# Kernel tuning notes

Hardware: AMD Instinct MI355X
Metric: run time of the kernel (lower is better)

## Reference

```python
import jax, jax.numpy as jnp
import numpy as np

N_HEAD = 8
DQK = 64
DV = 64
D_IN = 512
D_OUT = 512
D_MID = 2048
B = 4
L = 2048
EPS = 1e-5


def layernorm(x):
    mu = jnp.mean(x, axis=-1, keepdims=True)
    var = jnp.mean(jnp.square(x - mu), axis=-1, keepdims=True)
    return (x - mu) / jnp.sqrt(var + EPS)


def setup_inputs() -> dict:
    key = jax.random.key(0)
    ks = jax.random.split(key, 10)
    s = 0.02
    return {
        "query": jax.random.normal(ks[0], (B, L, D_IN), jnp.float32),
        "key": jax.random.normal(ks[1], (B, L, D_IN), jnp.float32),
        "value": jax.random.normal(ks[2], (B, L, D_IN), jnp.float32),
        "mask": jnp.zeros((B, L, L), jnp.float32),
        "WQ": jax.random.normal(ks[3], (D_IN, N_HEAD * DQK), jnp.float32) * s,
        "WK": jax.random.normal(ks[4], (D_IN, N_HEAD * DQK), jnp.float32) * s,
        "WV": jax.random.normal(ks[5], (D_IN, N_HEAD * DV), jnp.float32) * s,
        "WO": jax.random.normal(ks[6], (N_HEAD * DV, D_OUT), jnp.float32) * s,
        "W1": jax.random.normal(ks[7], (D_OUT, D_MID), jnp.float32) * s,
        "W2": jax.random.normal(ks[8], (D_MID, D_OUT), jnp.float32) * s,
    }


def reference(query, key, value, mask, WQ, WK, WV, WO, W1, W2):
    bsz = query.shape[0]
    # projections -> [b, h, l, d]
    Q = (query @ WQ).reshape(bsz, -1, N_HEAD, DQK).transpose(0, 2, 1, 3)
    K = (key @ WK).reshape(bsz, -1, N_HEAD, DQK).transpose(0, 2, 1, 3)
    V = (value @ WV).reshape(bsz, -1, N_HEAD, DV).transpose(0, 2, 1, 3)
    # scaled dot-product attention with additive mask [b, 1, lq, lk]
    scores = jnp.einsum("bhqd,bhkd->bhqk", Q, K) / jnp.sqrt(jnp.float32(DQK))
    w = jax.nn.softmax(scores + mask[:, None, :, :], axis=-1)
    out = jnp.einsum("bhqk,bhkd->bhqd", w, V)
    out = out.transpose(0, 2, 1, 3).reshape(bsz, -1, N_HEAD * DV)
    out = out @ WO
    out = layernorm(query + out)
    ff = jax.nn.relu(out @ W1) @ W2
    return layernorm(out + ff)
```

## Files before the change

kernel.cpp:

```cpp
#include <hip/hip_runtime.h>
#include <hip/hip_bf16.h>

using bf16 = __bf16;
typedef __bf16 bf16x4 __attribute__((ext_vector_type(4)));
typedef __bf16 bf16x8 __attribute__((ext_vector_type(8)));
typedef float f32x4 __attribute__((ext_vector_type(4)));

static constexpr int BATCH = 4;
static constexpr int SEQ   = 2048;
static constexpr int DIN   = 512;
static constexpr int NHEAD = 8;
static constexpr int DMID  = 2048;
static constexpr int MROWS = BATCH * SEQ;

__device__ __forceinline__ void gload16(const void* g, void* l)
{
    __builtin_amdgcn_global_load_lds(
        (const __attribute__((address_space(1))) unsigned int*)g,
        (__attribute__((address_space(3))) unsigned int*)l, 16, 0, 0);
}

__device__ __forceinline__ bf16x4 ds_tr16(const bf16* p)
{
    bf16x4 r;
    auto lp = (const __attribute__((address_space(3))) bf16*)p;
    asm volatile("ds_read_b64_tr_b16 %0, %1" : "=&v"(r) : "v"(lp) : "memory");
    return r;
}

__global__ __launch_bounds__(256) void tw_mask(
    const float* __restrict__ WQ, const float* __restrict__ WK,
    const float* __restrict__ WV, const float* __restrict__ WO,
    const float* __restrict__ W1, const float* __restrict__ W2,
    bf16* __restrict__ WQt, bf16* __restrict__ WKt, bf16* __restrict__ WVt,
    bf16* __restrict__ WOt, bf16* __restrict__ W1t, bf16* __restrict__ W2t,
    const float* __restrict__ q, const float* __restrict__ k,
    const float* __restrict__ v,
    bf16* __restrict__ qb, bf16* __restrict__ kb, bf16* __restrict__ vb,
    const uint4* __restrict__ mask, int* __restrict__ flag)
{
    const int bid = blockIdx.x;
    if (bid >= 4096) {
        const int idx = bid - 4096;
        const float* src = idx < 1024 ? q : idx < 2048 ? k : v;
        bf16*       dst = idx < 1024 ? qb : idx < 2048 ? kb : vb;
        const size_t b4 = (size_t)(idx & 1023) * 1024;
#pragma unroll
        for (int i = 0; i < 4; ++i) {
            const float4 f = reinterpret_cast<const float4*>(src)[b4 + i * 256 + threadIdx.x];
            bf16x4 h;
            h[0] = (bf16)f.x; h[1] = (bf16)f.y; h[2] = (bf16)f.z; h[3] = (bf16)f.w;
            reinterpret_cast<bf16x4*>(dst)[b4 + i * 256 + threadIdx.x] = h;
        }
        return;
    }
    if (bid >= 3072) {
        const uint4* p = mask + (size_t)(bid - 3072) * 4096;
        unsigned nz = 0;
#pragma unroll
        for (int i = 0; i < 16; ++i) {
            const uint4 u = p[i * 256 + threadIdx.x];
            nz |= u.x | u.y | u.z | u.w;
        }
        if (nz) atomicOr(flag, 1);
        return;
    }
    __shared__ float tile[32][33];
    const float* in; bf16* out; int ip, op, cx, ry;
    if (bid < 1024) {
        const int w = bid >> 8, idx = bid & 255;
        in  = w == 0 ? WQ  : w == 1 ? WK  : w == 2 ? WV  : WO;
        out = w == 0 ? WQt : w == 1 ? WKt : w == 2 ? WVt : WOt;
        ip = 512; op = 512; cx = idx & 15; ry = idx >> 4;
    } else if (bid < 2048) {
        const int idx = bid - 1024;
        in = W1; out = W1t; ip = 2048; op = 512; cx = idx & 63; ry = idx >> 6;
    } else {
        const int idx = bid - 2048;
        in = W2; out = W2t; ip = 512; op = 2048; cx = idx & 15; ry = idx >> 4;
    }
    const int c0 = cx * 32, r0 = ry * 32;
    const int tx = threadIdx.x & 31, ty = threadIdx.x >> 5;
    for (int i = 0; i < 32; i += 8)
        tile[ty + i][tx] = in[(size_t)(r0 + ty + i) * ip + c0 + tx];
    __syncthreads();
    for (int i = 0; i < 32; i += 8)
        out[(size_t)(c0 + ty + i) * op + r0 + tx] = (bf16)tile[tx][ty + i];
}

template <int ACT>
__global__ __launch_bounds__(256) void gemm128(const bf16* __restrict__ A,
                                               const bf16* __restrict__ Bt,
                                               bf16* __restrict__ C,
                                               int N, int K)
{
    __shared__ bf16 sA[128 * 64];
    __shared__ bf16 sB[128 * 64];

    const int t    = threadIdx.x;
    const int lane = t & 63;
    const int wave = t >> 6;
    const int wm   = wave >> 1;
    const int wn   = wave & 1;
    const int lr   = lane & 15;
    const int lq   = lane >> 4;

    const int m0 = blockIdx.y * 128;
    const int n0 = blockIdx.x * 128;

    const int srow = lane >> 3;
    const int scol = (lane & 7) * 8;

    f32x4 acc[4][4] = {};

    for (int k0 = 0; k0 < K; k0 += 64) {
        if (k0) __syncthreads();
#pragma unroll
        for (int i = 0; i < 4; ++i) {
            const int ch = wave * 4 + i;
            const int r  = ch * 8 + srow;
            gload16(A  + (size_t)(m0 + r) * K + k0 + scol, sA + ch * 512);
            gload16(Bt + (size_t)(n0 + r) * K + k0 + scol, sB + ch * 512);
        }
        __syncthreads();

#pragma unroll
        for (int kk = 0; kk < 2; ++kk) {
            bf16x8 af[4], bfr[4];
#pragma unroll
            for (int x = 0; x < 4; ++x) {
                af[x]  = *reinterpret_cast<const bf16x8*>(&sA[(wm * 64 + x * 16 + lr) * 64 + kk * 32 + lq * 8]);
                bfr[x] = *reinterpret_cast<const bf16x8*>(&sB[(wn * 64 + x * 16 + lr) * 64 + kk * 32 + lq * 8]);
            }
#pragma unroll
            for (int m = 0; m < 4; ++m)
#pragma unroll
                for (int n = 0; n < 4; ++n)
                    acc[m][n] = __builtin_amdgcn_mfma_f32_16x16x32_bf16(af[m], bfr[n], acc[m][n], 0, 0, 0);
        }
    }

#pragma unroll
    for (int n = 0; n < 4; ++n) {
        const int col = n0 + wn * 64 + n * 16 + lr;
#pragma unroll
        for (int m = 0; m < 4; ++m) {
            const int rowb = m0 + wm * 64 + m * 16 + lq * 4;
#pragma unroll
            for (int j = 0; j < 4; ++j) {
                float v = acc[m][n][j];
                if (ACT == 1) v = v > 0.f ? v : 0.f;
                C[(size_t)(rowb + j) * N + col] = (bf16)v;
            }
        }
    }
}

__global__ __launch_bounds__(256) void gemm64_qkvb(const bf16* __restrict__ qb,
                                                   const bf16* __restrict__ kb,
                                                   const bf16* __restrict__ vb,
                                                   const bf16* __restrict__ WQt,
                                                   const bf16* __restrict__ WKt,
                                                   const bf16* __restrict__ WVt,
                                                   bf16* __restrict__ Qb,
                                                   bf16* __restrict__ Kb,
                                                   bf16* __restrict__ Vt)
{
    __shared__ bf16 sA[64 * 64];
    __shared__ bf16 sB[128 * 64];

    const bf16* A  = blockIdx.z == 0 ? qb  : blockIdx.z == 1 ? kb  : vb;
    const bf16* Bt = blockIdx.z == 0 ? WQt : blockIdx.z == 1 ? WKt : WVt;
    const int K = DIN;

    const int t    = threadIdx.x;
    const int lane = t & 63;
    const int wave = t >> 6;
    const int lr   = lane & 15;
    const int lq   = lane >> 4;

    const int m0 = blockIdx.y * 64;
    const int n0 = blockIdx.x * 128;

    const int srow = lane >> 3;
    const int scol = (lane & 7) * 8;

    f32x4 acc[4][2] = {};

    for (int k0 = 0; k0 < K; k0 += 64) {
        if (k0) __syncthreads();
#pragma unroll
        for (int i = 0; i < 2; ++i) {
            const int ch = wave * 2 + i;
            gload16(A + (size_t)(m0 + ch * 8 + srow) * K + k0 + scol, sA + ch * 512);
        }
#pragma unroll
        for (int i = 0; i < 4; ++i) {
            const int ch = wave * 4 + i;
            gload16(Bt + (size_t)(n0 + ch * 8 + srow) * K + k0 + scol, sB + ch * 512);
        }
        __syncthreads();

#pragma unroll
        for (int kk = 0; kk < 2; ++kk) {
            bf16x8 af[4], bfr[2];
#pragma unroll
            for (int x = 0; x < 4; ++x)
                af[x] = *reinterpret_cast<const bf16x8*>(&sA[(x * 16 + lr) * 64 + kk * 32 + lq * 8]);
#pragma unroll
            for (int n = 0; n < 2; ++n)
                bfr[n] = *reinterpret_cast<const bf16x8*>(&sB[(wave * 32 + n * 16 + lr) * 64 + kk * 32 + lq * 8]);
#pragma unroll
            for (int m = 0; m < 4; ++m)
#pragma unroll
                for (int n = 0; n < 2; ++n)
                    acc[m][n] = __builtin_amdgcn_mfma_f32_16x16x32_bf16(af[m], bfr[n], acc[m][n], 0, 0, 0);
        }
    }

    if (blockIdx.z < 2) {
        bf16* C = blockIdx.z == 0 ? Qb : Kb;
#pragma unroll
        for (int n = 0; n < 2; ++n) {
            const int col = n0 + wave * 32 + n * 16 + lr;
#pragma unroll
            for (int m = 0; m < 4; ++m) {
                const int rowb = m0 + m * 16 + lq * 4;
#pragma unroll
                for (int j = 0; j < 4; ++j)
                    C[(size_t)(rowb + j) * DIN + col] = (bf16)acc[m][n][j];
            }
        }
    } else {
        __syncthreads();
#pragma unroll
        for (int n = 0; n < 2; ++n)
#pragma unroll
            for (int m = 0; m < 4; ++m)
#pragma unroll
                for (int j = 0; j < 4; ++j)
                    sB[(wave * 32 + n * 16 + lr) * 64 + m * 16 + lq * 4 + j] = (bf16)acc[m][n][j];
        __syncthreads();
        const int c = t >> 1, half = t & 1;
#pragma unroll
        for (int qq = 0; qq < 4; ++qq) {
            const bf16x8 vv = *reinterpret_cast<const bf16x8*>(&sB[c * 64 + half * 32 + qq * 8]);
            *reinterpret_cast<bf16x8*>(Vt + (size_t)(n0 + c) * MROWS + m0 + half * 32 + qq * 8) = vv;
        }
    }
}

__global__ __launch_bounds__(256) void attn_kernel(const bf16* __restrict__ Qb,
                                                   const bf16* __restrict__ Kb,
                                                   const bf16* __restrict__ Vt,
                                                   const float* __restrict__ mask,
                                                   bf16* __restrict__ O,
                                                   const int* __restrict__ mzf)
{
    const int bi   = blockIdx.x;
    const int xcd  = bi & 7;
    const int slot = bi >> 3;
    const int pair = xcd * 4 + (slot >> 4);
    const int qt   = slot & 15;
    const int h    = pair >> 2;
    const int b    = pair & 3;

    const int t    = threadIdx.x;
    const int lane = t & 63;
    const int wave = t >> 6;
    const int lr   = lane & 15;
    const int lq   = lane >> 4;
    const int q0   = qt * 128;
    const bool useM = (*mzf != 0);

    __shared__ bf16 sK[64 * 72];
    __shared__ bf16 sV[64 * 72];
    __shared__ bf16 sPT[4][2048];
    __shared__ bf16 sM[128 * 68];

    bf16x8 qf[2][2];
#pragma unroll
    for (int g = 0; g < 2; ++g) {
        const int qrow = q0 + wave * 32 + g * 16 + lr;
        const bf16* qp = Qb + (size_t)(b * SEQ + qrow) * DIN + h * 64 + lq * 8;
        qf[g][0] = *reinterpret_cast<const bf16x8*>(qp);
        qf[g][1] = *reinterpret_cast<const bf16x8*>(qp + 32);
    }

    f32x4 o[2][4] = {};
    f32x4 lrow[2] = {};

    const int sr = t >> 2;
    const int sc = (t & 3) << 3;

    const bf16*  kbase = Kb + (size_t)(b * SEQ) * DIN + h * 64;
    const bf16*  vbase = Vt + (size_t)(h * 64 + sr) * MROWS + b * SEQ;
    const float* mbase = mask + ((size_t)b * SEQ + q0) * SEQ;

    constexpr float L2E = 1.4426950408889634f;
    constexpr float SCL = 0.125f * L2E;
    const bf16x8 ones = {(bf16)1.f, (bf16)1.f, (bf16)1.f, (bf16)1.f,
                         (bf16)1.f, (bf16)1.f, (bf16)1.f, (bf16)1.f};

    int4 kr0 = *reinterpret_cast<const int4*>(kbase + (size_t)sr * DIN + sc);
    int4 kr1 = *reinterpret_cast<const int4*>(kbase + (size_t)sr * DIN + sc + 32);
    int4 vr0 = *reinterpret_cast<const int4*>(vbase + sc);
    int4 vr1 = *reinterpret_cast<const int4*>(vbase + sc + 32);

    for (int tile = 0; tile < SEQ / 64; ++tile) {
        if (tile) __syncthreads();

        *reinterpret_cast<int4*>(&sK[sr * 72 + sc])      = kr0;
        *reinterpret_cast<int4*>(&sK[sr * 72 + sc + 32]) = kr1;
        *reinterpret_cast<int4*>(&sV[sr * 72 + sc])      = vr0;
        *reinterpret_cast<int4*>(&sV[sr * 72 + sc + 32]) = vr1;
        if (useM) {
            const int k0 = tile * 64;
#pragma unroll
            for (int i = 0; i < 8; ++i) {
                const int idx = t + 256 * i;
                const float4 mr = *reinterpret_cast<const float4*>(
                    mbase + (size_t)(idx >> 4) * SEQ + k0 + (idx & 15) * 4);
                bf16x4 mv;
                mv[0] = (bf16)(mr.x * L2E); mv[1] = (bf16)(mr.y * L2E);
                mv[2] = (bf16)(mr.z * L2E); mv[3] = (bf16)(mr.w * L2E);
                *reinterpret_cast<bf16x4*>(&sM[(idx >> 4) * 68 + (idx & 15) * 4]) = mv;
            }
        }

        if (tile + 1 < SEQ / 64) {
            const int k0 = (tile + 1) * 64;
            kr0 = *reinterpret_cast<const int4*>(kbase + (size_t)(k0 + sr) * DIN + sc);
            kr1 = *reinterpret_cast<const int4*>(kbase + (size_t)(k0 + sr) * DIN + sc + 32);
            vr0 = *reinterpret_cast<const int4*>(vbase + k0 + sc);
            vr1 = *reinterpret_cast<const int4*>(vbase + k0 + sc + 32);
        }
        __syncthreads();

        bf16x8 kf[2][4];
#pragma unroll
        for (int s = 0; s < 2; ++s)
#pragma unroll
            for (int ni = 0; ni < 4; ++ni)
                kf[s][ni] = *reinterpret_cast<const bf16x8*>(&sK[(ni * 16 + lr) * 72 + s * 32 + lq * 8]);

#pragma unroll
        for (int g = 0; g < 2; ++g) {
            f32x4 sf[4] = {};
            __builtin_amdgcn_s_setprio(1);
#pragma unroll
            for (int s = 0; s < 2; ++s)
#pragma unroll
                for (int ni = 0; ni < 4; ++ni)
                    sf[ni] = __builtin_amdgcn_mfma_f32_16x16x32_bf16(qf[g][s], kf[s][ni], sf[ni], 0, 0, 0);
            __builtin_amdgcn_s_setprio(0);

#pragma unroll
            for (int ni = 0; ni < 4; ++ni) {
                bf16x4 pw;
                if (useM) {
#pragma unroll
                    for (int j = 0; j < 4; ++j) {
                        const float mval = (float)sM[(wave * 32 + g * 16 + lq * 4 + j) * 68 + ni * 16 + lr];
                        pw[j] = (bf16)exp2f(sf[ni][j] * SCL + mval);
                    }
                } else {
#pragma unroll
                    for (int j = 0; j < 4; ++j)
                        pw[j] = (bf16)exp2f(sf[ni][j] * SCL);
                }
                *reinterpret_cast<bf16x4*>(&sPT[wave][g * 1024 + (ni * 16 + lr) * 16 + lq * 4]) = pw;
            }
        }

        bf16x8 vfr[2][4];
#pragma unroll
        for (int s = 0; s < 2; ++s)
#pragma unroll
            for (int ni = 0; ni < 4; ++ni)
                vfr[s][ni] = *reinterpret_cast<const bf16x8*>(&sV[(ni * 16 + lr) * 72 + s * 32 + lq * 8]);

        asm volatile("s_waitcnt lgkmcnt(0)" ::: "memory");
        __builtin_amdgcn_sched_barrier(0);

#pragma unroll
        for (int g = 0; g < 2; ++g) {
            const bf16* pb = &sPT[wave][g * 1024 + lq * 128 + lr];
            const bf16x4 t00 = ds_tr16(pb);
            const bf16x4 t01 = ds_tr16(pb + 64);
            const bf16x4 t10 = ds_tr16(pb + 512);
            const bf16x4 t11 = ds_tr16(pb + 576);
            asm volatile("s_waitcnt lgkmcnt(0)" ::: "memory");
            __builtin_amdgcn_sched_barrier(0);
            const bf16x8 pa0 = __builtin_shufflevector(t00, t01, 0, 1, 2, 3, 4, 5, 6, 7);
            const bf16x8 pa1 = __builtin_shufflevector(t10, t11, 0, 1, 2, 3, 4, 5, 6, 7);

            __builtin_amdgcn_s_setprio(1);
            f32x4 rs = {};
            rs = __builtin_amdgcn_mfma_f32_16x16x32_bf16(pa0, ones, rs, 0, 0, 0);
#pragma unroll
            for (int ni = 0; ni < 4; ++ni)
                o[g][ni] = __builtin_amdgcn_mfma_f32_16x16x32_bf16(pa0, vfr[0][ni], o[g][ni], 0, 0, 0);
            rs = __builtin_amdgcn_mfma_f32_16x16x32_bf16(pa1, ones, rs, 0, 0, 0);
#pragma unroll
            for (int ni = 0; ni < 4; ++ni)
                o[g][ni] = __builtin_amdgcn_mfma_f32_16x16x32_bf16(pa1, vfr[1][ni], o[g][ni], 0, 0, 0);
            __builtin_amdgcn_s_setprio(0);
#pragma unroll
            for (int j = 0; j < 4; ++j)
                lrow[g][j] += rs[j];
        }
    }

#pragma unroll
    for (int g = 0; g < 2; ++g)
#pragma unroll
        for (int ni = 0; ni < 4; ++ni)
#pragma unroll
            for (int j = 0; j < 4; ++j) {
                const int row = q0 + wave * 32 + g * 16 + lq * 4 + j;
                const int col = h * 64 + ni * 16 + lr;
                O[(size_t)(b * SEQ + row) * DIN + col] = (bf16)(o[g][ni][j] / lrow[g][j]);
            }
}

__global__ __launch_bounds__(512) void gemm_ln(const bf16* __restrict__ A,
                                               const bf16* __restrict__ Bt,
                                               const float* __restrict__ X,
                                               bf16* __restrict__ Onb,
                                               float* __restrict__ Onf,
                                               int K)
{
    __shared__ bf16 sA[2][32 * 64];
    __shared__ bf16 sB[2][512 * 64];
    __shared__ float sRed[32][8];
    __shared__ float sMu[32];
    __shared__ float sRstd[32];

    const int t    = threadIdx.x;
    const int lane = t & 63;
    const int w    = t >> 6;
    const int lr   = lane & 15;
    const int lq   = lane >> 4;
    const int srow = lane >> 3;
    const int scol = (lane & 7) * 8;

    const int m0 = blockIdx.x * 32;

    auto stage = [&](int s, int b) {
        const int k0 = s * 64;
#pragma unroll
        for (int i = 0; i < 8; ++i) {
            const int ch = w * 8 + i;
            gload16(Bt + (size_t)(ch * 8 + srow) * K + k0 + scol, &sB[b][ch * 512]);
        }
        if (w < 4)
            gload16(A + (size_t)(m0 + w * 8 + srow) * K + k0 + scol, &sA[b][w * 512]);
    };

    f32x4 acc[2][4] = {};
    const int steps = K / 64;

    stage(0, 0);
    __syncthreads();

    for (int s = 0; s < steps; ++s) {
        const int b = s & 1;
        if (s + 1 < steps) stage(s + 1, b ^ 1);

#pragma unroll
        for (int kk = 0; kk < 2; ++kk) {
            bf16x8 af[2], bfr[4];
#pragma unroll
            for (int m = 0; m < 2; ++m)
                af[m] = *reinterpret_cast<const bf16x8*>(&sA[b][(m * 16 + lr) * 64 + kk * 32 + lq * 8]);
#pragma unroll
            for (int n = 0; n < 4; ++n)
                bfr[n] = *reinterpret_cast<const bf16x8*>(&sB[b][(w * 64 + n * 16 + lr) * 64 + kk * 32 + lq * 8]);
#pragma unroll
            for (int m = 0; m < 2; ++m)
#pragma unroll
                for (int n = 0; n < 4; ++n)
                    acc[m][n] = __builtin_amdgcn_mfma_f32_16x16x32_bf16(af[m], bfr[n], acc[m][n], 0, 0, 0);
        }
        __syncthreads();
    }

#pragma unroll
    for (int m = 0; m < 2; ++m)
#pragma unroll
        for (int n = 0; n < 4; ++n)
#pragma unroll
            for (int j = 0; j < 4; ++j)
                acc[m][n][j] += X[(size_t)(m0 + m * 16 + lq * 4 + j) * DIN + w * 64 + n * 16 + lr];

#pragma unroll
    for (int m = 0; m < 2; ++m)
#pragma unroll
        for (int j = 0; j < 4; ++j) {
            float s = acc[m][0][j] + acc[m][1][j] + acc[m][2][j] + acc[m][3][j];
            s += __shfl_xor(s, 1); s += __shfl_xor(s, 2);
            s += __shfl_xor(s, 4); s += __shfl_xor(s, 8);
            if (lr == 0) sRed[m * 16 + lq * 4 + j][w] = s;
        }
    __syncthreads();
    if (t < 32) {
        float s = 0.f;
#pragma unroll
        for (int ww = 0; ww < 8; ++ww) s += sRed[t][ww];
        sMu[t] = s * (1.f / DIN);
    }
    __syncthreads();

#pragma unroll
    for (int m = 0; m < 2; ++m)
#pragma unroll
        for (int j = 0; j < 4; ++j) {
            const float mu = sMu[m * 16 + lq * 4 + j];
            float s = 0.f;
#pragma unroll
            for (int n = 0; n < 4; ++n) {
                const float d = acc[m][n][j] - mu;
                s += d * d;
            }
            s += __shfl_xor(s, 1); s += __shfl_xor(s, 2);
            s += __shfl_xor(s, 4); s += __shfl_xor(s, 8);
            if (lr == 0) sRed[m * 16 + lq * 4 + j][w] = s;
        }
    __syncthreads();
    if (t < 32) {
        float s = 0.f;
#pragma unroll
        for (int ww = 0; ww < 8; ++ww) s += sRed[t][ww];
        sRstd[t] = rsqrtf(s * (1.f / DIN) + 1e-5f);
    }
    __syncthreads();

#pragma unroll
    for (int m = 0; m < 2; ++m)
#pragma unroll
        for (int j = 0; j < 4; ++j) {
            const int rl = m * 16 + lq * 4 + j;
            const float mu = sMu[rl], rstd = sRstd[rl];
            const size_t rowoff = (size_t)(m0 + rl) * DIN;
#pragma unroll
            for (int n = 0; n < 4; ++n) {
                const float r = (acc[m][n][j] - mu) * rstd;
                const int col = w * 64 + n * 16 + lr;
                if (Onb) Onb[rowoff + col] = (bf16)r;
                if (Onf) Onf[rowoff + col] = r;
            }
        }
}

extern "C" void kernel_launch(void* const* d_in, const int* in_sizes, int n_in,
                              void* d_out, int out_size, void* d_ws, size_t ws_size,
                              hipStream_t stream)
{
    const float* query = (const float*)d_in[0];
    const float* key   = (const float*)d_in[1];
    const float* value = (const float*)d_in[2];
    const float* mask  = (const float*)d_in[3];
    const float* WQ    = (const float*)d_in[4];
    const float* WK    = (const float*)d_in[5];
    const float* WV    = (const float*)d_in[6];
    const float* WO    = (const float*)d_in[7];
    const float* W1    = (const float*)d_in[8];
    const float* W2    = (const float*)d_in[9];

    char* w = (char*)d_ws;
    size_t off = 0;
    auto carve2 = [&](size_t elems) { bf16* p = (bf16*)(w + off); off += elems * 2; return p; };
    auto carve4 = [&](size_t elems) { float* p = (float*)(w + off); off += elems * 4; return p; };

    bf16* Qb    = carve2((size_t)MROWS * DIN);
    bf16* Kb    = carve2((size_t)MROWS * DIN);
    bf16* Vb    = carve2((size_t)MROWS * DIN);
    bf16* Vt    = carve2((size_t)MROWS * DIN);
    bf16* Mid   = carve2((size_t)MROWS * DMID);
    float* Ln1f = carve4((size_t)MROWS * DIN);
    bf16* WQt   = carve2((size_t)DIN * DIN);
    bf16* WKt   = carve2((size_t)DIN * DIN);
    bf16* WVt   = carve2((size_t)DIN * DIN);
    bf16* WOt   = carve2((size_t)DIN * DIN);
    bf16* W1t   = carve2((size_t)DIN * DMID);
    bf16* W2t   = carve2((size_t)DMID * DIN);
    int*  mzf   = (int*)(w + off); off += 16;
    if (off > ws_size) return;

    bf16* Ob   = Vb;
    bf16* Ln1b = Kb;
    bf16* qb = Mid;
    bf16* kb = Mid + (size_t)MROWS * DIN;
    bf16* vb = Mid + (size_t)2 * MROWS * DIN;

    const dim3 blk(256);

    hipMemsetAsync(mzf, 0, 4, stream);

    tw_mask<<<dim3(7168), blk, 0, stream>>>(WQ, WK, WV, WO, W1, W2,
                                            WQt, WKt, WVt, WOt, W1t, W2t,
                                            query, key, value, qb, kb, vb,
                                            (const uint4*)mask, mzf);

    gemm64_qkvb<<<dim3(DIN / 128, MROWS / 64, 3), blk, 0, stream>>>(qb, kb, vb,
                                                                    WQt, WKt, WVt, Qb, Kb, Vt);

    attn_kernel<<<dim3(512), blk, 0, stream>>>(Qb, Kb, Vt, mask, Ob, mzf);

    gemm_ln<<<dim3(MROWS / 32), dim3(512), 0, stream>>>(Ob, WOt, query, Ln1b, Ln1f, DIN);

    gemm128<1><<<dim3(DMID / 128, MROWS / 128), blk, 0, stream>>>(Ln1b, W1t, Mid, DMID, DIN);

    gemm_ln<<<dim3(MROWS / 32), dim3(512), 0, stream>>>(Mid, W2t, Ln1f,
                                                        (bf16*)nullptr, (float*)d_out, DMID);
}
```

Before: 376.3 us.

## Rework attention inner loop with 32x32 MFMA and register-resident P

The attention kernel moves from 16x16x32 MFMAs to 32x32x16 MFMAs and computes S transposed (K times Q), so the probabilities stay in registers. They are repacked with cvt_pk_bf16 and permlane32_swap instead of a round trip through LDS with transposed reads. K and V tiles use an XOR-swizzled shared layout instead of padding. Row sums are accumulated with scalar adds rather than an extra ones-MFMA, and the mask is read directly from global memory instead of being staged in LDS. This removes LDS traffic and waits per tile and lowers shared-memory use, at the cost of higher register pressure.

```diff
diff --git a/kernel.cpp b/kernel.cpp
--- a/kernel.cpp
+++ b/kernel.cpp
@@ -5,6 +5,8 @@
 typedef __bf16 bf16x4 __attribute__((ext_vector_type(4)));
 typedef __bf16 bf16x8 __attribute__((ext_vector_type(8)));
 typedef float f32x4 __attribute__((ext_vector_type(4)));
+typedef float f32x16 __attribute__((ext_vector_type(16)));
+typedef unsigned uint2v __attribute__((ext_vector_type(2)));
 
 static constexpr int BATCH = 4;
 static constexpr int SEQ   = 2048;
@@ -20,11 +22,10 @@
         (__attribute__((address_space(3))) unsigned int*)l, 16, 0, 0);
 }
 
-__device__ __forceinline__ bf16x4 ds_tr16(const bf16* p)
-{
-    bf16x4 r;
-    auto lp = (const __attribute__((address_space(3))) bf16*)p;
-    asm volatile("ds_read_b64_tr_b16 %0, %1" : "=&v"(r) : "v"(lp) : "memory");
+__device__ __forceinline__ unsigned cvtpk(float a, float b)
+{
+    unsigned r;
+    asm("v_cvt_pk_bf16_f32 %0, %1, %2" : "=v"(r) : "v"(a), "v"(b));
     return r;
 }
 
@@ -268,160 +269,138 @@
     const int t    = threadIdx.x;
     const int lane = t & 63;
     const int wave = t >> 6;
-    const int lr   = lane & 15;
-    const int lq   = lane >> 4;
+    const int l31  = lane & 31;
+    const int hi   = lane >> 5;
     const int q0   = qt * 128;
     const bool useM = (*mzf != 0);
 
-    __shared__ bf16 sK[64 * 72];
-    __shared__ bf16 sV[64 * 72];
-    __shared__ bf16 sPT[4][2048];
-    __shared__ bf16 sM[128 * 68];
-
-    bf16x8 qf[2][2];
-#pragma unroll
-    for (int g = 0; g < 2; ++g) {
-        const int qrow = q0 + wave * 32 + g * 16 + lr;
-        const bf16* qp = Qb + (size_t)(b * SEQ + qrow) * DIN + h * 64 + lq * 8;
-        qf[g][0] = *reinterpret_cast<const bf16x8*>(qp);
-        qf[g][1] = *reinterpret_cast<const bf16x8*>(qp + 32);
-    }
-
-    f32x4 o[2][4] = {};
-    f32x4 lrow[2] = {};
+    __shared__ bf16 sK[64 * 64];
+    __shared__ bf16 sV[64 * 64];
+    __shared__ float sL[4][32];
+
+    bf16x8 qf[4];
+#pragma unroll
+    for (int s = 0; s < 4; ++s)
+        qf[s] = *reinterpret_cast<const bf16x8*>(
+            Qb + (size_t)(b * SEQ + q0 + wave * 32 + l31) * DIN + h * 64 + s * 16 + hi * 8);
+
+    f32x16 o0 = {}, o1 = {};
+    float lacc = 0.f;
 
     const int sr = t >> 2;
-    const int sc = (t & 3) << 3;
-
-    const bf16*  kbase = Kb + (size_t)(b * SEQ) * DIN + h * 64;
-    const bf16*  vbase = Vt + (size_t)(h * 64 + sr) * MROWS + b * SEQ;
-    const float* mbase = mask + ((size_t)b * SEQ + q0) * SEQ;
+    const int c1 = t & 3;
+
+    const bf16* kbase = Kb + (size_t)(b * SEQ) * DIN + h * 64;
+    const bf16* vbase = Vt + (size_t)(h * 64 + sr) * MROWS + b * SEQ;
 
     constexpr float L2E = 1.4426950408889634f;
     constexpr float SCL = 0.125f * L2E;
-    const bf16x8 ones = {(bf16)1.f, (bf16)1.f, (bf16)1.f, (bf16)1.f,
-                         (bf16)1.f, (bf16)1.f, (bf16)1.f, (bf16)1.f};
-
-    int4 kr0 = *reinterpret_cast<const int4*>(kbase + (size_t)sr * DIN + sc);
-    int4 kr1 = *reinterpret_cast<const int4*>(kbase + (size_t)sr * DIN + sc + 32);
-    int4 vr0 = *reinterpret_cast<const int4*>(vbase + sc);
-    int4 vr1 = *reinterpret_cast<const int4*>(vbase + sc + 32);
+
+    int4 kr0 = *reinterpret_cast<const int4*>(kbase + (size_t)sr * DIN + c1 * 8);
+    int4 kr1 = *reinterpret_cast<const int4*>(kbase + (size_t)sr * DIN + c1 * 8 + 32);
+    int4 vr0 = *reinterpret_cast<const int4*>(vbase + c1 * 8);
+    int4 vr1 = *reinterpret_cast<const int4*>(vbase + c1 * 8 + 32);
 
     for (int tile = 0; tile < SEQ / 64; ++tile) {
         if (tile) __syncthreads();
 
-        *reinterpret_cast<int4*>(&sK[sr * 72 + sc])      = kr0;
-        *reinterpret_cast<int4*>(&sK[sr * 72 + sc + 32]) = kr1;
-        *reinterpret_cast<int4*>(&sV[sr * 72 + sc])      = vr0;
-        *reinterpret_cast<int4*>(&sV[sr * 72 + sc + 32]) = vr1;
-        if (useM) {
-            const int k0 = tile * 64;
-#pragma unroll
-            for (int i = 0; i < 8; ++i) {
-                const int idx = t + 256 * i;
-                const float4 mr = *reinterpret_cast<const float4*>(
-                    mbase + (size_t)(idx >> 4) * SEQ + k0 + (idx & 15) * 4);
-                bf16x4 mv;
-                mv[0] = (bf16)(mr.x * L2E); mv[1] = (bf16)(mr.y * L2E);
-                mv[2] = (bf16)(mr.z * L2E); mv[3] = (bf16)(mr.w * L2E);
-                *reinterpret_cast<bf16x4*>(&sM[(idx >> 4) * 68 + (idx & 15) * 4]) = mv;
-            }
+        {
+            const int x = sr & 7;
+            *reinterpret_cast<int4*>(&sK[sr * 64 + ((c1    ) ^ x) * 8]) = kr0;
+            *reinterpret_cast<int4*>(&sK[sr * 64 + ((c1 + 4) ^ x) * 8]) = kr1;
+            *reinterpret_cast<int4*>(&sV[sr * 64 + ((c1    ) ^ x) * 8]) = vr0;
+            *reinterpret_cast<int4*>(&sV[sr * 64 + ((c1 + 4) ^ x) * 8]) = vr1;
         }
 
         if (tile + 1 < SEQ / 64) {
             const int k0 = (tile + 1) * 64;
-            kr0 = *reinterpret_cast<const int4*>(kbase + (size_t)(k0 + sr) * DIN + sc);
-            kr1 = *reinterpret_cast<const int4*>(kbase + (size_t)(k0 + sr) * DIN + sc + 32);
-            vr0 = *reinterpret_cast<const int4*>(vbase + k0 + sc);
-            vr1 = *reinterpret_cast<const int4*>(vbase + k0 + sc + 32);
+            kr0 = *reinterpret_cast<const int4*>(kbase + (size_t)(k0 + sr) * DIN + c1 * 8);
+            kr1 = *reinterpret_cast<const int4*>(kbase + (size_t)(k0 + sr) * DIN + c1 * 8 + 32);
+            vr0 = *reinterpret_cast<const int4*>(vbase + k0 + c1 * 8);
+            vr1 = *reinterpret_cast<const int4*>(vbase + k0 + c1 * 8 + 32);
         }
         __syncthreads();
 
         bf16x8 kf[2][4];
 #pragma unroll
-        for (int s = 0; s < 2; ++s)
-#pragma unroll
-            for (int ni = 0; ni < 4; ++ni)
-                kf[s][ni] = *reinterpret_cast<const bf16x8*>(&sK[(ni * 16 + lr) * 72 + s * 32 + lq * 8]);
-
-#pragma unroll
-        for (int g = 0; g < 2; ++g) {
-            f32x4 sf[4] = {};
-            __builtin_amdgcn_s_setprio(1);
-#pragma unroll
-            for (int s = 0; s < 2; ++s)
-#pragma unroll
-                for (int ni = 0; ni < 4; ++ni)
-                    sf[ni] = __builtin_amdgcn_mfma_f32_16x16x32_bf16(qf[g][s], kf[s][ni], sf[ni], 0, 0, 0);
-            __builtin_amdgcn_s_setprio(0);
-
-#pragma unroll
-            for (int ni = 0; ni < 4; ++ni) {
-                bf16x4 pw;
-                if (useM) {
-#pragma unroll
-                    for (int j = 0; j < 4; ++j) {
-                        const float mval = (float)sM[(wave * 32 + g * 16 + lq * 4 + j) * 68 + ni * 16 + lr];
-                        pw[j] = (bf16)exp2f(sf[ni][j] * SCL + mval);
-                    }
-                } else {
-#pragma unroll
-                    for (int j = 0; j < 4; ++j)
-                        pw[j] = (bf16)exp2f(sf[ni][j] * SCL);
-                }
-                *reinterpret_cast<bf16x4*>(&sPT[wave][g * 1024 + (ni * 16 + lr) * 16 + lq * 4]) = pw;
-            }
-        }
-
-        bf16x8 vfr[2][4];
-#pragma unroll
-        for (int s = 0; s < 2; ++s)
-#pragma unroll
-            for (int ni = 0; ni < 4; ++ni)
-                vfr[s][ni] = *reinterpret_cast<const bf16x8*>(&sV[(ni * 16 + lr) * 72 + s * 32 + lq * 8]);
-
-        asm volatile("s_waitcnt lgkmcnt(0)" ::: "memory");
-        __builtin_amdgcn_sched_barrier(0);
-
-#pragma unroll
-        for (int g = 0; g < 2; ++g) {
-            const bf16* pb = &sPT[wave][g * 1024 + lq * 128 + lr];
-            const bf16x4 t00 = ds_tr16(pb);
-            const bf16x4 t01 = ds_tr16(pb + 64);
-            const bf16x4 t10 = ds_tr16(pb + 512);
-            const bf16x4 t11 = ds_tr16(pb + 576);
-            asm volatile("s_waitcnt lgkmcnt(0)" ::: "memory");
-            __builtin_amdgcn_sched_barrier(0);
-            const bf16x8 pa0 = __builtin_shufflevector(t00, t01, 0, 1, 2, 3, 4, 5, 6, 7);
-            const bf16x8 pa1 = __builtin_shufflevector(t10, t11, 0, 1, 2, 3, 4, 5, 6, 7);
-
-            __builtin_amdgcn_s_setprio(1);
-            f32x4 rs = {};
-            rs = __builtin_amdgcn_mfma_f32_16x16x32_bf16(pa0, ones, rs, 0, 0, 0);
-#pragma unroll
-            for (int ni = 0; ni < 4; ++ni)
-                o[g][ni] = __builtin_amdgcn_mfma_f32_16x16x32_bf16(pa0, vfr[0][ni], o[g][ni], 0, 0, 0);
-            rs = __builtin_amdgcn_mfma_f32_16x16x32_bf16(pa1, ones, rs, 0, 0, 0);
-#pragma unroll
-            for (int ni = 0; ni < 4; ++ni)
-                o[g][ni] = __builtin_amdgcn_mfma_f32_16x16x32_bf16(pa1, vfr[1][ni], o[g][ni], 0, 0, 0);
-            __builtin_amdgcn_s_setprio(0);
-#pragma unroll
-            for (int j = 0; j < 4; ++j)
-                lrow[g][j] += rs[j];
-        }
-    }
-
-#pragma unroll
-    for (int g = 0; g < 2; ++g)
-#pragma unroll
-        for (int ni = 0; ni < 4; ++ni)
-#pragma unroll
-            for (int j = 0; j < 4; ++j) {
-                const int row = q0 + wave * 32 + g * 16 + lq * 4 + j;
-                const int col = h * 64 + ni * 16 + lr;
-                O[(size_t)(b * SEQ + row) * DIN + col] = (bf16)(o[g][ni][j] / lrow[g][j]);
-            }
+        for (int kb = 0; kb < 2; ++kb)
+#pragma unroll
+            for (int s = 0; s < 4; ++s) {
+                const int r = kb * 32 + l31;
+                kf[kb][s] = *reinterpret_cast<const bf16x8*>(
+                    &sK[r * 64 + ((hi + 2 * s) ^ (r & 7)) * 8]);
+            }
+        bf16x8 vf[2][4];
+#pragma unroll
+        for (int dt = 0; dt < 2; ++dt)
+#pragma unroll
+            for (int c = 0; c < 4; ++c) {
+                const int r = dt * 32 + l31;
+                vf[dt][c] = *reinterpret_cast<const bf16x8*>(
+                    &sV[r * 64 + ((hi + 2 * c) ^ (r & 7)) * 8]);
+            }
+
+        f32x16 st0 = {}, st1 = {};
+#pragma unroll
+        for (int s = 0; s < 4; ++s) {
+            st0 = __builtin_amdgcn_mfma_f32_32x32x16_bf16(kf[0][s], qf[s], st0, 0, 0, 0);
+            st1 = __builtin_amdgcn_mfma_f32_32x32x16_bf16(kf[1][s], qf[s], st1, 0, 0, 0);
+        }
+
+        float p[32];
+        if (useM) {
+            const float* mrow = mask + ((size_t)(b * SEQ + q0 + wave * 32 + l31)) * SEQ + tile * 64;
+#pragma unroll
+            for (int r = 0; r < 16; ++r) {
+                const int kk = (r & 3) + 8 * (r >> 2) + 4 * hi;
+                p[r]      = exp2f(st0[r] * SCL + mrow[kk]      * L2E);
+                p[16 + r] = exp2f(st1[r] * SCL + mrow[32 + kk] * L2E);
+            }
+        } else {
+#pragma unroll
+            for (int r = 0; r < 16; ++r) {
+                p[r]      = exp2f(st0[r] * SCL);
+                p[16 + r] = exp2f(st1[r] * SCL);
+            }
+        }
+#pragma unroll
+        for (int r = 0; r < 32; ++r) lacc += p[r];
+
+        bf16x8 pa[4];
+#pragma unroll
+        for (int c = 0; c < 4; ++c) {
+            const int bse = c * 8;
+            unsigned u0 = cvtpk(p[bse + 0], p[bse + 1]);
+            unsigned u1 = cvtpk(p[bse + 2], p[bse + 3]);
+            unsigned u2 = cvtpk(p[bse + 4], p[bse + 5]);
+            unsigned u3 = cvtpk(p[bse + 6], p[bse + 7]);
+            const uint2v r02 = __builtin_amdgcn_permlane32_swap(u0, u2, false, false);
+            const uint2v r13 = __builtin_amdgcn_permlane32_swap(u1, u3, false, false);
+            union { unsigned u[4]; bf16x8 v; } pk;
+            pk.u[0] = r02.x; pk.u[1] = r13.x; pk.u[2] = r02.y; pk.u[3] = r13.y;
+            pa[c] = pk.v;
+        }
+
+#pragma unroll
+        for (int c = 0; c < 4; ++c) {
+            o0 = __builtin_amdgcn_mfma_f32_32x32x16_bf16(pa[c], vf[0][c], o0, 0, 0, 0);
+            o1 = __builtin_amdgcn_mfma_f32_32x32x16_bf16(pa[c], vf[1][c], o1, 0, 0, 0);
+        }
+    }
+
+    lacc += __shfl_xor(lacc, 32);
+    __syncthreads();
+    if (lane < 32) sL[wave][lane] = lacc;
+    __syncthreads();
+
+#pragma unroll
+    for (int r = 0; r < 16; ++r) {
+        const int qr = (r & 3) + 8 * (r >> 2) + 4 * hi;
+        const float inv = 1.f / sL[wave][qr];
+        const size_t rowoff = (size_t)(b * SEQ + q0 + wave * 32 + qr) * DIN + h * 64;
+        O[rowoff + l31]      = (bf16)(o0[r] * inv);
+        O[rowoff + 32 + l31] = (bf16)(o1[r] * inv);
+    }
 }
 
 __global__ __launch_bounds__(512) void gemm_ln(const bf16* __restrict__ A,
```

Measured after the change: 359.6 us. 4.4% less time.
